# Optimization experiments

Measured on AMD Instinct MI355X. Metric: run time of the kernel, lower is better.

The kernel has to match this reference:

```python
import jax, jax.numpy as jnp
import numpy as np

N = 2048        # reservoir_size
D_IN = 32       # input_dim
D_OUT = 16      # output_dim
H = 128         # PhysicsEncoder hidden_dim
B, T = 64, 256
LEAK = 0.3
CONNECTIVITY = 0.1
SPECTRAL_RADIUS = 0.95
LN_EPS = 1e-5


def setup_inputs() -> dict:
    key = jax.random.key(0)
    ks = jax.random.split(key, 24)
    x = jax.random.normal(ks[0], (B, T, D_IN), dtype=jnp.float32)
    # frozen input weights, input_scaling = 1.0
    W_in = jax.random.normal(ks[1], (N, D_IN), dtype=jnp.float32)
    # sparse reservoir, rescaled to spectral radius ~0.95 (analytic approx
    # rho ~ sigma*sqrt(N*p) for sparse gaussian, matches the torch rescale intent)
    mask = (jax.random.uniform(ks[2], (N, N)) < CONNECTIVITY).astype(jnp.float32)
    W_res = jax.random.normal(ks[3], (N, N), dtype=jnp.float32) * 0.1 * mask
    approx_radius = 0.1 * np.sqrt(N * CONNECTIVITY)
    W_res = W_res * (SPECTRAL_RADIUS / approx_radius)
    # attention: seq_len is always 1 inside the loop, so softmax over a length-1
    # axis is identically 1 and out == proj(v). Only the V slice of qkv matters.
    sc = 1.0 / np.sqrt(N)
    Wv = jax.random.uniform(ks[4], (N, N), minval=-sc, maxval=sc, dtype=jnp.float32)
    bv = jax.random.uniform(ks[5], (N,), minval=-sc, maxval=sc, dtype=jnp.float32)
    Wproj = jax.random.uniform(ks[6], (N, N), minval=-sc, maxval=sc, dtype=jnp.float32)
    bproj = jax.random.uniform(ks[7], (N,), minval=-sc, maxval=sc, dtype=jnp.float32)
    # physics encoder: Linear(N,H) -> LayerNorm -> GELU -> Linear(H,H) -> GELU -> Linear(H,N)
    s1 = 1.0 / np.sqrt(N)
    We1 = jax.random.uniform(ks[8], (H, N), minval=-s1, maxval=s1, dtype=jnp.float32)
    be1 = jax.random.uniform(ks[9], (H,), minval=-s1, maxval=s1, dtype=jnp.float32)
    ln_g = jnp.ones((H,), jnp.float32)
    ln_b = jnp.zeros((H,), jnp.float32)
    s2 = 1.0 / np.sqrt(H)
    We2 = jax.random.uniform(ks[10], (H, H), minval=-s2, maxval=s2, dtype=jnp.float32)
    be2 = jax.random.uniform(ks[11], (H,), minval=-s2, maxval=s2, dtype=jnp.float32)
    We3 = jax.random.uniform(ks[12], (N, H), minval=-s2, maxval=s2, dtype=jnp.float32)
    be3 = jax.random.uniform(ks[13], (N,), minval=-s2, maxval=s2, dtype=jnp.float32)
    # Bayesian output layer (reparameterized; epsilons passed in for determinism)
    s3 = 1.0 / np.sqrt(N)
    w_mu = jax.random.uniform(ks[14], (D_OUT, N), minval=-s3, maxval=s3, dtype=jnp.float32)
    w_rho = jnp.full((D_OUT, N), -3.0, jnp.float32)
    b_mu = jax.random.uniform(ks[15], (D_OUT,), minval=-s3, maxval=s3, dtype=jnp.float32)
    b_rho = jnp.full((D_OUT,), -3.0, jnp.float32)
    w_eps = jax.random.normal(ks[16], (D_OUT, N), dtype=jnp.float32)
    b_eps = jax.random.normal(ks[17], (D_OUT,), dtype=jnp.float32)
    return {
        "x": x, "W_in": W_in, "W_res": W_res,
        "Wv": Wv, "bv": bv, "Wproj": Wproj, "bproj": bproj,
        "We1": We1, "be1": be1, "ln_g": ln_g, "ln_b": ln_b,
        "We2": We2, "be2": be2, "We3": We3, "be3": be3,
        "w_mu": w_mu, "w_rho": w_rho, "b_mu": b_mu, "b_rho": b_rho,
        "w_eps": w_eps, "b_eps": b_eps,
    }


def _gelu(x):
    return jax.nn.gelu(x, approximate=False)  # torch nn.GELU default = exact erf


def reference(x, W_in, W_res, Wv, bv, Wproj, bproj,
              We1, be1, ln_g, ln_b, We2, be2, We3, be3,
              w_mu, w_rho, b_mu, b_rho, w_eps, b_eps):
    Bsz = x.shape[0]

    def step(states, x_t):
        # terms computed from PRE-attention state, as in the original loop order
        input_term = x_t @ W_in.T            # [B, N]
        reservoir_term = states @ W_res.T    # [B, N]
        # attention over a length-1 sequence: softmax == 1 -> out = proj(v)
        v = states @ Wv.T + bv
        s_att = v @ Wproj.T + bproj          # new `states` after attention
        # physics encoder on attended state
        h = s_att @ We1.T + be1
        mu = jnp.mean(h, axis=-1, keepdims=True)
        var = jnp.var(h, axis=-1, keepdims=True)
        h = (h - mu) * jax.lax.rsqrt(var + LN_EPS) * ln_g + ln_b
        h = _gelu(h)
        h = _gelu(h @ We2.T + be2)
        phys = h @ We3.T + be3               # [B, N]
        new_state = (1.0 - LEAK) * s_att + LEAK * jnp.tanh(
            input_term + reservoir_term + phys)
        return new_state, None

    s0 = jnp.zeros((Bsz, N), x.dtype)
    final_state, _ = jax.lax.scan(step, s0, jnp.swapaxes(x, 0, 1))  # scan over T

    # Bayesian output layer (reparameterization with fixed eps)
    w_sigma = jnp.log1p(jnp.exp(w_rho))
    b_sigma = jnp.log1p(jnp.exp(b_rho))
    weight = w_mu + w_sigma * w_eps
    bias = b_mu + b_sigma * b_eps
    predictions = final_state @ weight.T + bias  # [B, D_OUT]
    return predictions
```

## Files before the change

### kernel.cpp

```cpp
#include <hip/hip_runtime.h>
#include <hip/hip_fp16.h>
#include <cstdint>
#include <cstddef>

typedef _Float16 f16x8 __attribute__((ext_vector_type(8)));
typedef float    f32x4 __attribute__((ext_vector_type(4)));

#define MFMA(A,B,C) __builtin_amdgcn_mfma_f32_16x16x32_f16((A),(B),(C),0,0,0)

#define NRES  2048
#define DIN   32
#define DOUT  16
#define HDIM  128
#define BBATCH 64
#define TSTEPS 256
#define WCOLS 4224
#define NBLK_W 264
#define NBLK  265

#define OFF_WBIG  ((size_t)0)
#define OFF_BIAS  ((size_t)17301504)
#define OFF_WE2H  ((size_t)17318400)
#define OFF_WE3H  ((size_t)17351168)
#define OFF_S16   ((size_t)17875456)
#define OFF_YP    ((size_t)18137600)
#define OFF_WINH  ((size_t)19219200)
#define OFF_CNT   ((size_t)19350272)

__device__ __forceinline__ float gelu_exact(float v) {
  return 0.5f * v * (1.0f + erff(v * 0.70710678118654752f));
}

__device__ __forceinline__ void stg_f32(float* p, float v) {
  __hip_atomic_store((unsigned*)p, __builtin_bit_cast(unsigned, v),
                     __ATOMIC_RELAXED, __HIP_MEMORY_SCOPE_AGENT);
}
__device__ __forceinline__ void stg_f16(_Float16* p, _Float16 v) {
  __hip_atomic_store((unsigned short*)p, __builtin_bit_cast(unsigned short, v),
                     __ATOMIC_RELAXED, __HIP_MEMORY_SCOPE_AGENT);
}


__global__ void k_cast(const float* __restrict__ src, _Float16* __restrict__ dst, int n) {
  int i = blockIdx.x * blockDim.x + threadIdx.x;
  int stride = gridDim.x * blockDim.x;
  for (; i < n; i += stride) dst[i] = (_Float16)src[i];
}

__global__ void k_batt(const float* __restrict__ Wproj, const float* __restrict__ bv,
                       const float* __restrict__ bproj, float* __restrict__ bias_big) {
  int c = blockIdx.x, tid = threadIdx.x;
  float p = 0.f;
  for (int k = tid; k < NRES; k += 256) p += Wproj[(size_t)c * NRES + k] * bv[k];
  for (int m = 1; m < 64; m <<= 1) p += __shfl_xor(p, m);
  __shared__ float r4[4];
  if ((tid & 63) == 0) r4[tid >> 6] = p;
  __syncthreads();
  if (tid == 0) bias_big[2048 + c] = r4[0] + r4[1] + r4[2] + r4[3] + bproj[c];
}

__global__ void k_bh1(const float* __restrict__ We1, const float* __restrict__ be1,
                      float* __restrict__ bias_big) {
  int h = blockIdx.x, tid = threadIdx.x;
  float p = 0.f;
  for (int n = tid; n < NRES; n += 256) p += We1[(size_t)h * NRES + n] * bias_big[2048 + n];
  for (int m = 1; m < 64; m <<= 1) p += __shfl_xor(p, m);
  __shared__ float r4[4];
  if ((tid & 63) == 0) r4[tid >> 6] = p;
  __syncthreads();
  if (tid == 0) bias_big[4096 + h] = r4[0] + r4[1] + r4[2] + r4[3] + be1[h];
}

__global__ void __launch_bounds__(256) k_gemm1(const float* __restrict__ Wproj,
                                               const float* __restrict__ Wv,
                                               _Float16* __restrict__ wbig) {
  __shared__ _Float16 BT[64][40];
  const int kblock = blockIdx.x, cblock = blockIdx.y;
  const int tid = threadIdx.x, wv = tid >> 6, lane = tid & 63;
  const int l4 = lane >> 4, l15 = lane & 15;
  const int crow0 = cblock * 64 + wv * 16;
  f32x4 acc[4];
  f32x4 zero = {0.f, 0.f, 0.f, 0.f};
  for (int i = 0; i < 4; ++i) acc[i] = zero;

  for (int mc = 0; mc < 64; ++mc) {
    const int m0 = mc * 32;
    {
      int m = tid >> 3, kk = (tid & 7) * 8;
      const float* src = &Wv[(size_t)(m0 + m) * NRES + kblock * 64 + kk];
      float4 v0 = *(const float4*)src;
      float4 v1 = *(const float4*)(src + 4);
      float tmp[8] = {v0.x, v0.y, v0.z, v0.w, v1.x, v1.y, v1.z, v1.w};
      #pragma unroll
      for (int j = 0; j < 8; ++j) BT[kk + j][m] = (_Float16)tmp[j];
    }
    __syncthreads();
    const float* pa = &Wproj[(size_t)(crow0 + l15) * NRES + m0 + l4 * 8];
    float4 a0 = *(const float4*)pa;
    float4 a1 = *(const float4*)(pa + 4);
    f16x8 af;
    af[0]=(_Float16)a0.x; af[1]=(_Float16)a0.y; af[2]=(_Float16)a0.z; af[3]=(_Float16)a0.w;
    af[4]=(_Float16)a1.x; af[5]=(_Float16)a1.y; af[6]=(_Float16)a1.z; af[7]=(_Float16)a1.w;
    #pragma unroll
    for (int kt = 0; kt < 4; ++kt) {
      f16x8 bf = *(const f16x8*)&BT[kt * 16 + l15][l4 * 8];
      acc[kt] = MFMA(af, bf, acc[kt]);
    }
    __syncthreads();
  }
  #pragma unroll
  for (int kt = 0; kt < 4; ++kt)
    #pragma unroll
    for (int i = 0; i < 4; ++i) {
      int c = crow0 + l4 * 4 + i;
      int k = kblock * 64 + kt * 16 + l15;
      wbig[(size_t)(2048 + c) * NRES + k] = (_Float16)acc[kt][i];
    }
}

__global__ void __launch_bounds__(256) k_gemm2(const float* __restrict__ We1,
                                               _Float16* __restrict__ wbig) {
  __shared__ _Float16 BT[64][40];
  const int kblock = blockIdx.x, hblock = blockIdx.y;
  const int tid = threadIdx.x, wv = tid >> 6, lane = tid & 63;
  const int l4 = lane >> 4, l15 = lane & 15;
  const int hrow0 = hblock * 64 + wv * 16;
  f32x4 acc[4];
  f32x4 zero = {0.f, 0.f, 0.f, 0.f};
  for (int i = 0; i < 4; ++i) acc[i] = zero;

  for (int nc = 0; nc < 64; ++nc) {
    const int n0 = nc * 32;
    {
      int n = tid >> 3, kk = (tid & 7) * 8;
      f16x8 v = *(const f16x8*)&wbig[(size_t)(2048 + n0 + n) * NRES + kblock * 64 + kk];
      #pragma unroll
      for (int j = 0; j < 8; ++j) BT[kk + j][n] = v[j];
    }
    __syncthreads();
    const float* pa = &We1[(size_t)(hrow0 + l15) * NRES + n0 + l4 * 8];
    float4 a0 = *(const float4*)pa;
    float4 a1 = *(const float4*)(pa + 4);
    f16x8 af;
    af[0]=(_Float16)a0.x; af[1]=(_Float16)a0.y; af[2]=(_Float16)a0.z; af[3]=(_Float16)a0.w;
    af[4]=(_Float16)a1.x; af[5]=(_Float16)a1.y; af[6]=(_Float16)a1.z; af[7]=(_Float16)a1.w;
    #pragma unroll
    for (int kt = 0; kt < 4; ++kt) {
      f16x8 bf = *(const f16x8*)&BT[kt * 16 + l15][l4 * 8];
      acc[kt] = MFMA(af, bf, acc[kt]);
    }
    __syncthreads();
  }
  #pragma unroll
  for (int kt = 0; kt < 4; ++kt)
    #pragma unroll
    for (int i = 0; i < 4; ++i) {
      int h = hrow0 + l4 * 4 + i;
      int k = kblock * 64 + kt * 16 + l15;
      wbig[(size_t)(4096 + h) * NRES + k] = (_Float16)acc[kt][i];
    }
}

__device__ __forceinline__ void gbar3(unsigned* slots, unsigned* wake, int b, unsigned phase) {
  asm volatile("s_waitcnt vmcnt(0)" ::: "memory");
  __syncthreads();
  if (threadIdx.x == 0) {
    __hip_atomic_store(slots + b, phase, __ATOMIC_RELAXED, __HIP_MEMORY_SCOPE_AGENT);
    unsigned spins = 0;
    while (__hip_atomic_load(wake + (size_t)b * 16, __ATOMIC_RELAXED, __HIP_MEMORY_SCOPE_AGENT) < phase) {
      __builtin_amdgcn_s_sleep(1);
      if (++spins > (1u << 20)) break;
    }
    (void)__hip_atomic_load(wake + (size_t)b * 16, __ATOMIC_ACQUIRE, __HIP_MEMORY_SCOPE_AGENT);
  }
  __syncthreads();
}


__global__ void __launch_bounds__(256, 2) k_main(
    const float* __restrict__ x,
    const float* __restrict__ ln_g, const float* __restrict__ ln_b,
    const float* __restrict__ be2v, const float* __restrict__ be3v,
    const float* __restrict__ w_mu, const float* __restrict__ w_rho,
    const float* __restrict__ b_mu, const float* __restrict__ b_rho,
    const float* __restrict__ w_eps, const float* __restrict__ b_eps,
    const _Float16* __restrict__ wbig, const float* __restrict__ bias_big,
    const _Float16* __restrict__ we2h, const _Float16* __restrict__ we3h,
    const _Float16* __restrict__ winh,
    _Float16* s16, float* yp,
    unsigned* cnt, float* __restrict__ out)
{
  const int b = blockIdx.x, tid = threadIdx.x;
  unsigned* slots = cnt;
  unsigned* wake  = cnt + 512;

  if (b == NBLK_W) {
    if (tid >= 64) return;
    for (unsigned p = 1; p <= 2u * TSTEPS; ++p) {
      unsigned spins = 0;
      for (;;) {
        bool ok = true;
        #pragma unroll
        for (int j = 0; j < 5; ++j) {
          unsigned v = __hip_atomic_load(slots + tid + j * 64, __ATOMIC_RELAXED, __HIP_MEMORY_SCOPE_AGENT);
          ok = ok && (v >= p);
        }
        if (__all((int)ok)) break;
        if (++spins > (1u << 19)) break;
        __builtin_amdgcn_s_sleep(1);
      }
      #pragma unroll
      for (int j = 0; j < 5; ++j) {
        int blk = tid + j * 64;
        if (blk < NBLK_W)
          __hip_atomic_store(wake + (size_t)blk * 16, p, __ATOMIC_RELAXED, __HIP_MEMORY_SCOPE_AGENT);
      }
    }
    return;
  }

  const int wv = tid >> 6, lane = tid & 63;
  const int l4 = lane >> 4, l15 = lane & 15;

  __shared__ float    lds_red[4][64][17];
  __shared__ _Float16 lds_w2[128][136];
  __shared__ _Float16 lds_h1[16][136];
  __shared__ _Float16 lds_g2[16][136];
  __shared__ _Float16 lds_x[16][40];

  const int strip = b;
  f16x8 Bf[16];
  #pragma unroll
  for (int ks = 0; ks < 16; ++ks)
    Bf[ks] = *(const f16x8*)&wbig[(size_t)(strip * 16 + l15) * NRES + wv * 512 + ks * 32 + l4 * 8];

  const bool doS3 = (b < 256);
  const int R0 = (b >> 6) * 16, C0 = (b & 63) * 32;

  float g8[8], bb8[8], bh8[8];
  #pragma unroll
  for (int jj = 0; jj < 8; ++jj) {
    g8[jj]  = ln_g[l15 + 16 * jj];
    bb8[jj] = ln_b[l15 + 16 * jj];
    bh8[jj] = bias_big[4096 + l15 + 16 * jj];
  }
  float be2r[2];
  #pragma unroll
  for (int ct = 0; ct < 2; ++ct) be2r[ct] = be2v[(wv * 2 + ct) * 16 + l15];

  const int mycol = C0 + wv * 16 + l15;
  f16x8 We3f[4];
  f16x8 Winf;
  float be3r = 0.f, battr = 0.f;
  if (doS3 && wv < 2) {
    #pragma unroll
    for (int ks = 0; ks < 4; ++ks)
      We3f[ks] = *(const f16x8*)&we3h[(size_t)mycol * HDIM + ks * 32 + l4 * 8];
    be3r  = be3v[mycol];
    battr = bias_big[2048 + mycol];
    Winf  = *(const f16x8*)&winh[(size_t)mycol * DIN + l4 * 8];
  }

  {
    int row = tid >> 1, half = tid & 1;
    #pragma unroll
    for (int j = 0; j < 8; ++j) {
      f16x8 v = *(const f16x8*)&we2h[(size_t)row * HDIM + half * 64 + j * 8];
      *(f16x8*)&lds_w2[row][half * 64 + j * 8] = v;
    }
  }
  __syncthreads();

  const f32x4 zero = {0.f, 0.f, 0.f, 0.f};
  unsigned phase = 0;

  for (int t = 0; t < TSTEPS; ++t) {
    f32x4 a0 = zero, a1 = zero, a2 = zero, a3 = zero;
    #pragma unroll
    for (int ks = 0; ks < 16; ++ks) {
      const int kk = wv * 512 + ks * 32 + l4 * 8;
      f16x8 A0 = *(const f16x8*)&s16[(size_t)(l15) * NRES + kk];
      f16x8 A1 = *(const f16x8*)&s16[(size_t)(16 + l15) * NRES + kk];
      f16x8 A2 = *(const f16x8*)&s16[(size_t)(32 + l15) * NRES + kk];
      f16x8 A3 = *(const f16x8*)&s16[(size_t)(48 + l15) * NRES + kk];
      a0 = MFMA(A0, Bf[ks], a0);
      a1 = MFMA(A1, Bf[ks], a1);
      a2 = MFMA(A2, Bf[ks], a2);
      a3 = MFMA(A3, Bf[ks], a3);
    }
    #pragma unroll
    for (int i = 0; i < 4; ++i) {
      lds_red[wv][lane][0 + i]  = a0[i];
      lds_red[wv][lane][4 + i]  = a1[i];
      lds_red[wv][lane][8 + i]  = a2[i];
      lds_red[wv][lane][12 + i] = a3[i];
    }
    __syncthreads();
    #pragma unroll
    for (int i = 0; i < 4; ++i) {
      float s = lds_red[0][lane][wv * 4 + i] + lds_red[1][lane][wv * 4 + i]
              + lds_red[2][lane][wv * 4 + i] + lds_red[3][lane][wv * 4 + i];
      stg_f32(&yp[(size_t)(wv * 16 + l4 * 4 + i) * WCOLS + strip * 16 + l15], s);
    }
    ++phase;
    gbar3(slots, wake, b, phase);

    if (doS3) {
      {
        int xr = tid >> 4, k0 = (tid & 15) * 2;
        const float* xs = &x[((size_t)(R0 + xr) * TSTEPS + t) * DIN + k0];
        lds_x[xr][k0]     = (_Float16)xs[0];
        lds_x[xr][k0 + 1] = (_Float16)xs[1];
      }
      const int lr = wv * 4 + l4;
      float h1v[8], s1 = 0.f, s2 = 0.f;
      const size_t yb = (size_t)(R0 + lr) * WCOLS + 4096;
      #pragma unroll
      for (int jj = 0; jj < 8; ++jj) {
        float v = yp[yb + l15 + 16 * jj] + bh8[jj];
        h1v[jj] = v; s1 += v; s2 += v * v;
      }
      #pragma unroll
      for (int m = 1; m < 16; m <<= 1) { s1 += __shfl_xor(s1, m); s2 += __shfl_xor(s2, m); }
      const float mu = s1 * (1.f / 128.f);
      const float var = s2 * (1.f / 128.f) - mu * mu;
      const float rs = rsqrtf(var + 1e-5f);
      #pragma unroll
      for (int jj = 0; jj < 8; ++jj) {
        float hn = (h1v[jj] - mu) * rs * g8[jj] + bb8[jj];
        lds_h1[lr][l15 + 16 * jj] = (_Float16)gelu_exact(hn);
      }
      __syncthreads();
      f32x4 c0 = zero, c1 = zero;
      #pragma unroll
      for (int ks = 0; ks < 4; ++ks) {
        f16x8 af = *(const f16x8*)&lds_h1[l15][ks * 32 + l4 * 8];
        f16x8 b0 = *(const f16x8*)&lds_w2[(wv * 2 + 0) * 16 + l15][ks * 32 + l4 * 8];
        f16x8 b1 = *(const f16x8*)&lds_w2[(wv * 2 + 1) * 16 + l15][ks * 32 + l4 * 8];
        c0 = MFMA(af, b0, c0);
        c1 = MFMA(af, b1, c1);
      }
      #pragma unroll
      for (int i = 0; i < 4; ++i) {
        int rr = l4 * 4 + i;
        lds_g2[rr][(wv * 2 + 0) * 16 + l15] = (_Float16)gelu_exact(c0[i] + be2r[0]);
        lds_g2[rr][(wv * 2 + 1) * 16 + l15] = (_Float16)gelu_exact(c1[i] + be2r[1]);
      }
      __syncthreads();
      if (wv < 2) {
        f32x4 accp = zero;
        #pragma unroll
        for (int ks = 0; ks < 4; ++ks) {
          f16x8 af = *(const f16x8*)&lds_g2[l15][ks * 32 + l4 * 8];
          accp = MFMA(af, We3f[ks], accp);
        }
        f16x8 ax = *(const f16x8*)&lds_x[l15][l4 * 8];
        f32x4 acci = MFMA(ax, Winf, zero);
        #pragma unroll
        for (int i = 0; i < 4; ++i) {
          int r2 = l4 * 4 + i, grow = R0 + r2;
          float satt = yp[(size_t)grow * WCOLS + 2048 + mycol] + battr;
          float rrv  = yp[(size_t)grow * WCOLS + mycol];
          float ns = 0.7f * satt + 0.3f * tanhf(acci[i] + rrv + accp[i] + be3r);
          stg_f16(&s16[(size_t)grow * NRES + mycol], (_Float16)ns);
        }
      }
    }
    ++phase;
    gbar3(slots, wake, b, phase);
  }

  if (b < BBATCH) {
    float* red = &lds_red[0][0][0];
    int o = tid >> 4, sg = tid & 15;
    float p = 0.f;
    for (int n = sg * 128; n < sg * 128 + 128; ++n) {
      float sv = (float)s16[(size_t)b * NRES + n];
      float w = w_mu[(size_t)o * NRES + n]
              + log1pf(expf(w_rho[(size_t)o * NRES + n])) * w_eps[(size_t)o * NRES + n];
      p += sv * w;
    }
    red[o * 17 + sg] = p;
    __syncthreads();
    if (tid < DOUT) {
      float sum = 0.f;
      for (int q = 0; q < 16; ++q) sum += red[tid * 17 + q];
      float bs = b_mu[tid] + log1pf(expf(b_rho[tid])) * b_eps[tid];
      out[b * DOUT + tid] = sum + bs;
    }
  }
}


extern "C" void kernel_launch(void* const* d_in, const int* in_sizes, int n_in,
                              void* d_out, int out_size, void* d_ws, size_t ws_size,
                              hipStream_t stream) {
  (void)in_sizes; (void)n_in; (void)out_size; (void)ws_size;
  const float* x     = (const float*)d_in[0];
  const float* W_in  = (const float*)d_in[1];
  const float* W_res = (const float*)d_in[2];
  const float* Wv    = (const float*)d_in[3];
  const float* bv    = (const float*)d_in[4];
  const float* Wproj = (const float*)d_in[5];
  const float* bproj = (const float*)d_in[6];
  const float* We1   = (const float*)d_in[7];
  const float* be1   = (const float*)d_in[8];
  const float* ln_g  = (const float*)d_in[9];
  const float* ln_b  = (const float*)d_in[10];
  const float* We2   = (const float*)d_in[11];
  const float* be2   = (const float*)d_in[12];
  const float* We3   = (const float*)d_in[13];
  const float* be3   = (const float*)d_in[14];
  const float* w_mu  = (const float*)d_in[15];
  const float* w_rho = (const float*)d_in[16];
  const float* b_mu  = (const float*)d_in[17];
  const float* b_rho = (const float*)d_in[18];
  const float* w_eps = (const float*)d_in[19];
  const float* b_eps = (const float*)d_in[20];
  float* out = (float*)d_out;

  char* ws = (char*)d_ws;
  _Float16* wbig     = (_Float16*)(ws + OFF_WBIG);
  float*    bias_big = (float*)(ws + OFF_BIAS);
  _Float16* we2h     = (_Float16*)(ws + OFF_WE2H);
  _Float16* we3h     = (_Float16*)(ws + OFF_WE3H);
  _Float16* s16      = (_Float16*)(ws + OFF_S16);
  float*    yp       = (float*)(ws + OFF_YP);
  _Float16* winh     = (_Float16*)(ws + OFF_WINH);
  unsigned* cnt      = (unsigned*)(ws + OFF_CNT);

  hipMemsetAsync(bias_big, 0, WCOLS * sizeof(float), stream);
  hipMemsetAsync(s16, 0, (size_t)BBATCH * NRES * sizeof(_Float16), stream);
  hipMemsetAsync(cnt, 0, 264 * 4, stream);
  hipMemsetAsync((char*)cnt + 264 * 4, 0xFF, 56 * 4, stream);
  hipMemsetAsync(cnt + 512, 0, 264 * 64, stream);

  k_cast<<<4096, 256, 0, stream>>>(W_res, wbig, NRES * NRES);
  k_cast<<<64,   256, 0, stream>>>(We2, we2h, HDIM * HDIM);
  k_cast<<<1024, 256, 0, stream>>>(We3, we3h, NRES * HDIM);
  k_cast<<<256,  256, 0, stream>>>(W_in, winh, NRES * DIN);
  k_batt<<<NRES, 256, 0, stream>>>(Wproj, bv, bproj, bias_big);
  k_gemm1<<<dim3(32, 32), 256, 0, stream>>>(Wproj, Wv, wbig);
  k_bh1<<<HDIM, 256, 0, stream>>>(We1, be1, bias_big);
  k_gemm2<<<dim3(32, 2), 256, 0, stream>>>(We1, wbig);

  k_main<<<NBLK, 256, 0, stream>>>(x, ln_g, ln_b, be2, be3,
                                   w_mu, w_rho, b_mu, b_rho, w_eps, b_eps,
                                   wbig, bias_big, we2h, we3h, winh, s16, yp, cnt, out);
}
```

Before: 7.290 ms.

## Fold encoder-first-layer strips into first 8 blocks and vectorize global stores

Removes the 8 extra persistent blocks that handled the We1-fused strips. The first 8 worker blocks now compute a second MFMA accumulation from a separate wh1 buffer, so the grid shrinks to 256 workers plus one barrier waker and every worker does stage 3. Per-element scalar atomic stores of yp and s16 are replaced by 16-byte global stores with sc0 sc1 bits, staged through LDS. This cuts the number of blocks participating in each grid barrier and reduces store count. In exchange, the first 8 blocks carry extra loads and MFMAs on every step, which creates a load imbalance.

```diff
diff --git a/kernel.cpp b/kernel.cpp
--- a/kernel.cpp
+++ b/kernel.cpp
@@ -15,29 +15,25 @@
 #define BBATCH 64
 #define TSTEPS 256
 #define WCOLS 4224
-#define NBLK_W 264
-#define NBLK  265
+#define NWORK 256
+#define NBLK  257
 
 #define OFF_WBIG  ((size_t)0)
+#define OFF_WH1   ((size_t)16777216)
 #define OFF_BIAS  ((size_t)17301504)
 #define OFF_WE2H  ((size_t)17318400)
 #define OFF_WE3H  ((size_t)17351168)
 #define OFF_S16   ((size_t)17875456)
 #define OFF_YP    ((size_t)18137600)
 #define OFF_WINH  ((size_t)19219200)
-#define OFF_CNT   ((size_t)19350272)
+#define OFF_CNT   ((size_t)19350528)
 
 __device__ __forceinline__ float gelu_exact(float v) {
   return 0.5f * v * (1.0f + erff(v * 0.70710678118654752f));
 }
 
-__device__ __forceinline__ void stg_f32(float* p, float v) {
-  __hip_atomic_store((unsigned*)p, __builtin_bit_cast(unsigned, v),
-                     __ATOMIC_RELAXED, __HIP_MEMORY_SCOPE_AGENT);
-}
-__device__ __forceinline__ void stg_f16(_Float16* p, _Float16 v) {
-  __hip_atomic_store((unsigned short*)p, __builtin_bit_cast(unsigned short, v),
-                     __ATOMIC_RELAXED, __HIP_MEMORY_SCOPE_AGENT);
+__device__ __forceinline__ void stg16(void* p, f32x4 v) {
+  asm volatile("global_store_dwordx4 %0, %1, off sc0 sc1" :: "v"(p), "v"(v) : "memory");
 }
 
 
@@ -119,7 +115,8 @@
 }
 
 __global__ void __launch_bounds__(256) k_gemm2(const float* __restrict__ We1,
-                                               _Float16* __restrict__ wbig) {
+                                               const _Float16* __restrict__ wbig,
+                                               _Float16* __restrict__ wh1) {
   __shared__ _Float16 BT[64][40];
   const int kblock = blockIdx.x, hblock = blockIdx.y;
   const int tid = threadIdx.x, wv = tid >> 6, lane = tid & 63;
@@ -157,7 +154,7 @@
     for (int i = 0; i < 4; ++i) {
       int h = hrow0 + l4 * 4 + i;
       int k = kblock * 64 + kt * 16 + l15;
-      wbig[(size_t)(4096 + h) * NRES + k] = (_Float16)acc[kt][i];
+      wh1[(size_t)h * NRES + k] = (_Float16)acc[kt][i];
     }
 }
 
@@ -184,7 +181,8 @@
     const float* __restrict__ w_mu, const float* __restrict__ w_rho,
     const float* __restrict__ b_mu, const float* __restrict__ b_rho,
     const float* __restrict__ w_eps, const float* __restrict__ b_eps,
-    const _Float16* __restrict__ wbig, const float* __restrict__ bias_big,
+    const _Float16* __restrict__ wbig, const _Float16* __restrict__ wh1,
+    const float* __restrict__ bias_big,
     const _Float16* __restrict__ we2h, const _Float16* __restrict__ we3h,
     const _Float16* __restrict__ winh,
     _Float16* s16, float* yp,
@@ -194,14 +192,14 @@
   unsigned* slots = cnt;
   unsigned* wake  = cnt + 512;
 
-  if (b == NBLK_W) {
+  if (b == NWORK) {
     if (tid >= 64) return;
     for (unsigned p = 1; p <= 2u * TSTEPS; ++p) {
       unsigned spins = 0;
       for (;;) {
         bool ok = true;
         #pragma unroll
-        for (int j = 0; j < 5; ++j) {
+        for (int j = 0; j < 4; ++j) {
           unsigned v = __hip_atomic_load(slots + tid + j * 64, __ATOMIC_RELAXED, __HIP_MEMORY_SCOPE_AGENT);
           ok = ok && (v >= p);
         }
@@ -210,11 +208,8 @@
         __builtin_amdgcn_s_sleep(1);
       }
       #pragma unroll
-      for (int j = 0; j < 5; ++j) {
-        int blk = tid + j * 64;
-        if (blk < NBLK_W)
-          __hip_atomic_store(wake + (size_t)blk * 16, p, __ATOMIC_RELAXED, __HIP_MEMORY_SCOPE_AGENT);
-      }
+      for (int j = 0; j < 4; ++j)
+        __hip_atomic_store(wake + (size_t)(tid + j * 64) * 16, p, __ATOMIC_RELAXED, __HIP_MEMORY_SCOPE_AGENT);
     }
     return;
   }
@@ -227,14 +222,15 @@
   __shared__ _Float16 lds_h1[16][136];
   __shared__ _Float16 lds_g2[16][136];
   __shared__ _Float16 lds_x[16][40];
-
-  const int strip = b;
+  __shared__ _Float16 lds_ns[16][40];
+
+  const bool dual = (b < 8);
   f16x8 Bf[16];
   #pragma unroll
   for (int ks = 0; ks < 16; ++ks)
-    Bf[ks] = *(const f16x8*)&wbig[(size_t)(strip * 16 + l15) * NRES + wv * 512 + ks * 32 + l4 * 8];
-
-  const bool doS3 = (b < 256);
+    Bf[ks] = *(const f16x8*)&wbig[(size_t)(b * 16 + l15) * NRES + wv * 512 + ks * 32 + l4 * 8];
+  const _Float16* wh1p = &wh1[(size_t)(b * 16 + l15) * NRES + wv * 512 + l4 * 8];
+
   const int R0 = (b >> 6) * 16, C0 = (b & 63) * 32;
 
   float g8[8], bb8[8], bh8[8];
@@ -252,7 +248,7 @@
   f16x8 We3f[4];
   f16x8 Winf;
   float be3r = 0.f, battr = 0.f;
-  if (doS3 && wv < 2) {
+  if (wv < 2) {
     #pragma unroll
     for (int ks = 0; ks < 4; ++ks)
       We3f[ks] = *(const f16x8*)&we3h[(size_t)mycol * HDIM + ks * 32 + l4 * 8];
@@ -274,8 +270,13 @@
   const f32x4 zero = {0.f, 0.f, 0.f, 0.f};
   unsigned phase = 0;
 
+  const int cr  = tid >> 2, cch = tid & 3;
+  const int rqi = (cr >> 4) * 4 + (cr & 3);
+  const int pl4 = (cr >> 2) & 3;
+
   for (int t = 0; t < TSTEPS; ++t) {
     f32x4 a0 = zero, a1 = zero, a2 = zero, a3 = zero;
+    f32x4 e0 = zero, e1 = zero, e2 = zero, e3 = zero;
     #pragma unroll
     for (int ks = 0; ks < 16; ++ks) {
       const int kk = wv * 512 + ks * 32 + l4 * 8;
@@ -287,6 +288,13 @@
       a1 = MFMA(A1, Bf[ks], a1);
       a2 = MFMA(A2, Bf[ks], a2);
       a3 = MFMA(A3, Bf[ks], a3);
+      if (dual) {
+        f16x8 Bx = *(const f16x8*)&wh1p[ks * 32];
+        e0 = MFMA(A0, Bx, e0);
+        e1 = MFMA(A1, Bx, e1);
+        e2 = MFMA(A2, Bx, e2);
+        e3 = MFMA(A3, Bx, e3);
+      }
     }
     #pragma unroll
     for (int i = 0; i < 4; ++i) {
@@ -296,75 +304,102 @@
       lds_red[wv][lane][12 + i] = a3[i];
     }
     __syncthreads();
-    #pragma unroll
-    for (int i = 0; i < 4; ++i) {
-      float s = lds_red[0][lane][wv * 4 + i] + lds_red[1][lane][wv * 4 + i]
-              + lds_red[2][lane][wv * 4 + i] + lds_red[3][lane][wv * 4 + i];
-      stg_f32(&yp[(size_t)(wv * 16 + l4 * 4 + i) * WCOLS + strip * 16 + l15], s);
+    {
+      f32x4 v;
+      #pragma unroll
+      for (int c = 0; c < 4; ++c) {
+        int pl = pl4 * 16 + cch * 4 + c;
+        v[c] = lds_red[0][pl][rqi] + lds_red[1][pl][rqi]
+             + lds_red[2][pl][rqi] + lds_red[3][pl][rqi];
+      }
+      stg16(&yp[(size_t)cr * WCOLS + b * 16 + cch * 4], v);
+    }
+    if (dual) {
+      __syncthreads();
+      #pragma unroll
+      for (int i = 0; i < 4; ++i) {
+        lds_red[wv][lane][0 + i]  = e0[i];
+        lds_red[wv][lane][4 + i]  = e1[i];
+        lds_red[wv][lane][8 + i]  = e2[i];
+        lds_red[wv][lane][12 + i] = e3[i];
+      }
+      __syncthreads();
+      f32x4 v2;
+      #pragma unroll
+      for (int c = 0; c < 4; ++c) {
+        int pl = pl4 * 16 + cch * 4 + c;
+        v2[c] = lds_red[0][pl][rqi] + lds_red[1][pl][rqi]
+              + lds_red[2][pl][rqi] + lds_red[3][pl][rqi];
+      }
+      stg16(&yp[(size_t)cr * WCOLS + 4096 + b * 16 + cch * 4], v2);
     }
     ++phase;
     gbar3(slots, wake, b, phase);
 
-    if (doS3) {
-      {
-        int xr = tid >> 4, k0 = (tid & 15) * 2;
-        const float* xs = &x[((size_t)(R0 + xr) * TSTEPS + t) * DIN + k0];
-        lds_x[xr][k0]     = (_Float16)xs[0];
-        lds_x[xr][k0 + 1] = (_Float16)xs[1];
-      }
-      const int lr = wv * 4 + l4;
-      float h1v[8], s1 = 0.f, s2 = 0.f;
-      const size_t yb = (size_t)(R0 + lr) * WCOLS + 4096;
-      #pragma unroll
-      for (int jj = 0; jj < 8; ++jj) {
-        float v = yp[yb + l15 + 16 * jj] + bh8[jj];
-        h1v[jj] = v; s1 += v; s2 += v * v;
-      }
-      #pragma unroll
-      for (int m = 1; m < 16; m <<= 1) { s1 += __shfl_xor(s1, m); s2 += __shfl_xor(s2, m); }
-      const float mu = s1 * (1.f / 128.f);
-      const float var = s2 * (1.f / 128.f) - mu * mu;
-      const float rs = rsqrtf(var + 1e-5f);
-      #pragma unroll
-      for (int jj = 0; jj < 8; ++jj) {
-        float hn = (h1v[jj] - mu) * rs * g8[jj] + bb8[jj];
-        lds_h1[lr][l15 + 16 * jj] = (_Float16)gelu_exact(hn);
-      }
-      __syncthreads();
-      f32x4 c0 = zero, c1 = zero;
+    {
+      int xr = tid >> 4, k0 = (tid & 15) * 2;
+      const float* xs = &x[((size_t)(R0 + xr) * TSTEPS + t) * DIN + k0];
+      lds_x[xr][k0]     = (_Float16)xs[0];
+      lds_x[xr][k0 + 1] = (_Float16)xs[1];
+    }
+    const int lr = wv * 4 + l4;
+    float h1v[8], s1 = 0.f, s2 = 0.f;
+    const size_t yb = (size_t)(R0 + lr) * WCOLS + 4096;
+    #pragma unroll
+    for (int jj = 0; jj < 8; ++jj) {
+      float v = yp[yb + l15 + 16 * jj] + bh8[jj];
+      h1v[jj] = v; s1 += v; s2 += v * v;
+    }
+    #pragma unroll
+    for (int m = 1; m < 16; m <<= 1) { s1 += __shfl_xor(s1, m); s2 += __shfl_xor(s2, m); }
+    const float mu = s1 * (1.f / 128.f);
+    const float var = s2 * (1.f / 128.f) - mu * mu;
+    const float rs = rsqrtf(var + 1e-5f);
+    #pragma unroll
+    for (int jj = 0; jj < 8; ++jj) {
+      float hn = (h1v[jj] - mu) * rs * g8[jj] + bb8[jj];
+      lds_h1[lr][l15 + 16 * jj] = (_Float16)gelu_exact(hn);
+    }
+    __syncthreads();
+    f32x4 c0 = zero, c1 = zero;
+    #pragma unroll
+    for (int ks = 0; ks < 4; ++ks) {
+      f16x8 af = *(const f16x8*)&lds_h1[l15][ks * 32 + l4 * 8];
+      f16x8 b0 = *(const f16x8*)&lds_w2[(wv * 2 + 0) * 16 + l15][ks * 32 + l4 * 8];
+      f16x8 b1 = *(const f16x8*)&lds_w2[(wv * 2 + 1) * 16 + l15][ks * 32 + l4 * 8];
+      c0 = MFMA(af, b0, c0);
+      c1 = MFMA(af, b1, c1);
+    }
+    #pragma unroll
+    for (int i = 0; i < 4; ++i) {
+      int rr = l4 * 4 + i;
+      lds_g2[rr][(wv * 2 + 0) * 16 + l15] = (_Float16)gelu_exact(c0[i] + be2r[0]);
+      lds_g2[rr][(wv * 2 + 1) * 16 + l15] = (_Float16)gelu_exact(c1[i] + be2r[1]);
+    }
+    __syncthreads();
+    if (wv < 2) {
+      f32x4 accp = zero;
       #pragma unroll
       for (int ks = 0; ks < 4; ++ks) {
-        f16x8 af = *(const f16x8*)&lds_h1[l15][ks * 32 + l4 * 8];
-        f16x8 b0 = *(const f16x8*)&lds_w2[(wv * 2 + 0) * 16 + l15][ks * 32 + l4 * 8];
-        f16x8 b1 = *(const f16x8*)&lds_w2[(wv * 2 + 1) * 16 + l15][ks * 32 + l4 * 8];
-        c0 = MFMA(af, b0, c0);
-        c1 = MFMA(af, b1, c1);
-      }
+        f16x8 af = *(const f16x8*)&lds_g2[l15][ks * 32 + l4 * 8];
+        accp = MFMA(af, We3f[ks], accp);
+      }
+      f16x8 ax = *(const f16x8*)&lds_x[l15][l4 * 8];
+      f32x4 acci = MFMA(ax, Winf, zero);
       #pragma unroll
       for (int i = 0; i < 4; ++i) {
-        int rr = l4 * 4 + i;
-        lds_g2[rr][(wv * 2 + 0) * 16 + l15] = (_Float16)gelu_exact(c0[i] + be2r[0]);
-        lds_g2[rr][(wv * 2 + 1) * 16 + l15] = (_Float16)gelu_exact(c1[i] + be2r[1]);
-      }
-      __syncthreads();
-      if (wv < 2) {
-        f32x4 accp = zero;
-        #pragma unroll
-        for (int ks = 0; ks < 4; ++ks) {
-          f16x8 af = *(const f16x8*)&lds_g2[l15][ks * 32 + l4 * 8];
-          accp = MFMA(af, We3f[ks], accp);
-        }
-        f16x8 ax = *(const f16x8*)&lds_x[l15][l4 * 8];
-        f32x4 acci = MFMA(ax, Winf, zero);
-        #pragma unroll
-        for (int i = 0; i < 4; ++i) {
-          int r2 = l4 * 4 + i, grow = R0 + r2;
-          float satt = yp[(size_t)grow * WCOLS + 2048 + mycol] + battr;
-          float rrv  = yp[(size_t)grow * WCOLS + mycol];
-          float ns = 0.7f * satt + 0.3f * tanhf(acci[i] + rrv + accp[i] + be3r);
-          stg_f16(&s16[(size_t)grow * NRES + mycol], (_Float16)ns);
-        }
-      }
+        int r2 = l4 * 4 + i;
+        float satt = yp[(size_t)(R0 + r2) * WCOLS + 2048 + mycol] + battr;
+        float rrv  = yp[(size_t)(R0 + r2) * WCOLS + mycol];
+        float ns = 0.7f * satt + 0.3f * tanhf(acci[i] + rrv + accp[i] + be3r);
+        lds_ns[r2][wv * 16 + l15] = (_Float16)ns;
+      }
+    }
+    __syncthreads();
+    if (tid < 64) {
+      int r = tid >> 2, ch = tid & 3;
+      f16x8 v = *(const f16x8*)&lds_ns[r][ch * 8];
+      stg16(&s16[(size_t)(R0 + r) * NRES + C0 + ch * 8], __builtin_bit_cast(f32x4, v));
     }
     ++phase;
     gbar3(slots, wake, b, phase);
@@ -421,6 +456,7 @@
 
   char* ws = (char*)d_ws;
   _Float16* wbig     = (_Float16*)(ws + OFF_WBIG);
+  _Float16* wh1      = (_Float16*)(ws + OFF_WH1);
   float*    bias_big = (float*)(ws + OFF_BIAS);
   _Float16* we2h     = (_Float16*)(ws + OFF_WE2H);
   _Float16* we3h     = (_Float16*)(ws + OFF_WE3H);
@@ -431,9 +467,7 @@
 
   hipMemsetAsync(bias_big, 0, WCOLS * sizeof(float), stream);
   hipMemsetAsync(s16, 0, (size_t)BBATCH * NRES * sizeof(_Float16), stream);
-  hipMemsetAsync(cnt, 0, 264 * 4, stream);
-  hipMemsetAsync((char*)cnt + 264 * 4, 0xFF, 56 * 4, stream);
-  hipMemsetAsync(cnt + 512, 0, 264 * 64, stream);
+  hipMemsetAsync(cnt, 0, 512 * 4 + 256 * 64, stream);
 
   k_cast<<<4096, 256, 0, stream>>>(W_res, wbig, NRES * NRES);
   k_cast<<<64,   256, 0, stream>>>(We2, we2h, HDIM * HDIM);
@@ -442,9 +476,9 @@
   k_batt<<<NRES, 256, 0, stream>>>(Wproj, bv, bproj, bias_big);
   k_gemm1<<<dim3(32, 32), 256, 0, stream>>>(Wproj, Wv, wbig);
   k_bh1<<<HDIM, 256, 0, stream>>>(We1, be1, bias_big);
-  k_gemm2<<<dim3(32, 2), 256, 0, stream>>>(We1, wbig);
+  k_gemm2<<<dim3(32, 2), 256, 0, stream>>>(We1, wbig, wh1);
 
   k_main<<<NBLK, 256, 0, stream>>>(x, ln_g, ln_b, be2, be3,
                                    w_mu, w_rho, b_mu, b_rho, w_eps, b_eps,
-                                   wbig, bias_big, we2h, we3h, winh, s16, yp, cnt, out);
-}
+                                   wbig, wh1, bias_big, we2h, we3h, winh, s16, yp, cnt, out);
+}
```

After: 6.630 ms. 1.1x faster.
